# Kernel tuning notes

Hardware: AMD Instinct MI355X
Metric: run time of the kernel (lower is better)

## Reference

```python
import jax, jax.numpy as jnp
import numpy as np

W_WORDS = 30  # hardcoded by `temp[i][30*j+k]` in the original module


def setup_inputs() -> dict:
    key = jax.random.key(0)
    k1, k2 = jax.random.split(key)
    input_var = jax.random.randint(k1, (32, 32, W_WORDS), 0, 50000, dtype=jnp.int64)
    W_emb = jax.random.normal(k2, (50000, 300), dtype=jnp.float32)
    return {"input_var": input_var, "W_emb": W_emb}


def reference(input_var, W_emb):
    B, S, W = input_var.shape
    E = W_emb.shape[1]

    mask3 = input_var != 0                               # [B,S,W]
    word_mask = mask3.reshape(-1, W).astype(jnp.uint8)   # [B*S, W]
    sent_mask = (mask3.sum(axis=2) != 0).astype(jnp.uint8)  # [B,S]

    # Vectorized version of the triple loop: keep tokens up to the FIRST zero
    # in each sentence (the loop `break`s on the first zero), zero the rest.
    keep = jnp.cumprod(mask3.astype(jnp.int32), axis=2).astype(bool)  # [B,S,W]
    temp = jnp.where(keep, input_var, 0).reshape(B, S * W)            # [B, S*W]
    mask = (temp != 0).astype(jnp.uint8)                              # [B, S*W]

    # model_type == 'word' branch; dropout p=0 is identity
    embedded = W_emb[input_var].reshape(-1, W, E)   # [B*S, W, E]
    share_enc_embedded = W_emb[temp]                # [B, S*W, E]

    return embedded, share_enc_embedded, mask, word_mask, sent_mask
```

## Files before the change

### kernel.cpp

```cpp
#include <hip/hip_runtime.h>

constexpr int B  = 32;
constexpr int S  = 32;
constexpr int W  = 30;
constexpr int E  = 300;
constexpr int EV = E / 4;
constexpr int NSENT = B * S;
constexpr int NTOK  = NSENT * W;
constexpr int NF4   = NTOK * EV;

constexpr long OFF_EMB   = 0;
constexpr long OFF_SHARE = (long)NTOK * E;
constexpr long OFF_MASK  = OFF_SHARE + (long)NTOK * E;
constexpr long OFF_WM    = OFF_MASK + (long)NTOK;
constexpr long OFF_SM    = OFF_WM + (long)NTOK;

__global__ __launch_bounds__(256) void prep_kernel(
    const int* __restrict__ input,
    float* __restrict__ out,
    int* __restrict__ zarr)
{
    const int sent = blockIdx.x * 256 + threadIdx.x;
    if (sent >= NSENT) return;

    int vals[W];
    #pragma unroll
    for (int k = 0; k < W; ++k) vals[k] = input[sent * W + k];

    int z = W, any = 0;
    #pragma unroll
    for (int k = 0; k < W; ++k) {
        any |= (vals[k] != 0);
        if (vals[k] == 0 && z == W) z = k;
    }

    zarr[sent] = z;
    out[OFF_SM + sent] = any ? 1.0f : 0.0f;

    #pragma unroll
    for (int k = 0; k < W; ++k) {
        out[OFF_WM   + (long)sent * W + k] = (vals[k] != 0) ? 1.0f : 0.0f;
        out[OFF_MASK + (long)sent * W + k] = (k < z) ? 1.0f : 0.0f;
    }
}

__global__ __launch_bounds__(256) void gather_kernel(
    const int* __restrict__ input,
    const int* __restrict__ zarr,
    const float* __restrict__ Wemb,
    float* __restrict__ out)
{
    const int g = blockIdx.x * 256 + threadIdx.x;

    const int token = g / EV;
    const int q     = g - token * EV;
    const int sent  = token / W;
    const int k     = token - sent * W;

    const int idx = input[token];
    const int z   = zarr[sent];
    const int tix = (k < z) ? idx : 0;

    const float4* __restrict__ W4 = (const float4*)Wemb;
    float4 a = W4[(long)idx * EV + q];
    float4 b = (tix == idx) ? a : W4[(long)q];

    ((float4*)(out + OFF_EMB))[g]   = a;
    ((float4*)(out + OFF_SHARE))[g] = b;
}

extern "C" void kernel_launch(void* const* d_in, const int* in_sizes, int n_in,
                              void* d_out, int out_size, void* d_ws, size_t ws_size,
                              hipStream_t stream) {
    const int*   input = (const int*)d_in[0];
    const float* Wemb  = (const float*)d_in[1];
    float*       out   = (float*)d_out;
    int*         zarr  = (int*)d_ws;

    prep_kernel<<<(NSENT + 255) / 256, 256, 0, stream>>>(input, out, zarr);
    gather_kernel<<<NF4 / 256, 256, 0, stream>>>(input, zarr, Wemb, out);
}
```

Measured before the change: 121.6 us.

## Fuse mask prep into gather kernel with per-sentence blocks and wave ballot

Merges the mask/prefix computation kernel into the embedding gather kernel. Each block handles one ninth of a sentence, computes the first-zero position with a wavefront ballot, stages token indices in shared memory, and part 0 writes the mask outputs. This removes a second launch, the serial per-thread prep loop, and the workspace round trip. In exchange, every block re-reads the sentence indices and pays a barrier, and 6 of 256 threads per block sit idle.

```diff
diff --git a/kernel.cpp b/kernel.cpp
--- a/kernel.cpp
+++ b/kernel.cpp
@@ -7,7 +7,8 @@
 constexpr int EV = E / 4;
 constexpr int NSENT = B * S;
 constexpr int NTOK  = NSENT * W;
-constexpr int NF4   = NTOK * EV;
+constexpr int PARTS = 9;
+constexpr int F4_PER_PART = (W * EV) / PARTS;
 
 constexpr long OFF_EMB   = 0;
 constexpr long OFF_SHARE = (long)NTOK * E;
@@ -15,55 +16,53 @@
 constexpr long OFF_WM    = OFF_MASK + (long)NTOK;
 constexpr long OFF_SM    = OFF_WM + (long)NTOK;
 
-__global__ __launch_bounds__(256) void prep_kernel(
+__global__ __launch_bounds__(256) void fused_kernel(
     const int* __restrict__ input,
-    float* __restrict__ out,
-    int* __restrict__ zarr)
-{
-    const int sent = blockIdx.x * 256 + threadIdx.x;
-    if (sent >= NSENT) return;
-
-    int vals[W];
-    #pragma unroll
-    for (int k = 0; k < W; ++k) vals[k] = input[sent * W + k];
-
-    int z = W, any = 0;
-    #pragma unroll
-    for (int k = 0; k < W; ++k) {
-        any |= (vals[k] != 0);
-        if (vals[k] == 0 && z == W) z = k;
-    }
-
-    zarr[sent] = z;
-    out[OFF_SM + sent] = any ? 1.0f : 0.0f;
-
-    #pragma unroll
-    for (int k = 0; k < W; ++k) {
-        out[OFF_WM   + (long)sent * W + k] = (vals[k] != 0) ? 1.0f : 0.0f;
-        out[OFF_MASK + (long)sent * W + k] = (k < z) ? 1.0f : 0.0f;
-    }
-}
-
-__global__ __launch_bounds__(256) void gather_kernel(
-    const int* __restrict__ input,
-    const int* __restrict__ zarr,
     const float* __restrict__ Wemb,
     float* __restrict__ out)
 {
-    const int g = blockIdx.x * 256 + threadIdx.x;
+    const int bid  = blockIdx.x;
+    const int sent = bid / PARTS;
+    const int part = bid - sent * PARTS;
+    const int tid  = threadIdx.x;
 
-    const int token = g / EV;
-    const int q     = g - token * EV;
-    const int sent  = token / W;
-    const int k     = token - sent * W;
+    __shared__ int idx_s[W];
+    __shared__ int tix_s[W];
 
-    const int idx = input[token];
-    const int z   = zarr[sent];
-    const int tix = (k < z) ? idx : 0;
+    if (tid < 64) {
+        const int k = tid;
+        const int v = (k < W) ? input[sent * W + k] : 1;
+        const unsigned long long bz = __ballot(v == 0);
+        const int z = bz ? (int)__builtin_ctzll(bz) : W;
+        if (k < W) {
+            idx_s[k] = v;
+            tix_s[k] = (k < z) ? v : 0;
+            if (part == 0) {
+                out[OFF_WM   + (long)sent * W + k] = (v != 0) ? 1.0f : 0.0f;
+                out[OFF_MASK + (long)sent * W + k] = (k < z) ? 1.0f : 0.0f;
+            }
+        }
+        if (part == 0 && k == 0) {
+            constexpr unsigned long long ALLZ = (1ull << W) - 1;
+            out[OFF_SM + sent] = (bz != ALLZ) ? 1.0f : 0.0f;
+        }
+    }
+    __syncthreads();
+
+    if (tid >= F4_PER_PART) return;
+
+    const int i = part * F4_PER_PART + tid;
+    const int k = i / EV;
+    const int q = i - k * EV;
+
+    const int idx = idx_s[k];
+    const int tix = tix_s[k];
 
     const float4* __restrict__ W4 = (const float4*)Wemb;
+    const long g = (long)sent * (W * EV) + i;
+
     float4 a = W4[(long)idx * EV + q];
-    float4 b = (tix == idx) ? a : W4[(long)q];
+    float4 b = (tix == idx) ? a : W4[q];
 
     ((float4*)(out + OFF_EMB))[g]   = a;
     ((float4*)(out + OFF_SHARE))[g] = b;
@@ -75,8 +74,6 @@
     const int*   input = (const int*)d_in[0];
     const float* Wemb  = (const float*)d_in[1];
     float*       out   = (float*)d_out;
-    int*         zarr  = (int*)d_ws;
 
-    prep_kernel<<<(NSENT + 255) / 256, 256, 0, stream>>>(input, out, zarr);
-    gather_kernel<<<NF4 / 256, 256, 0, stream>>>(input, zarr, Wemb, out);
+    fused_kernel<<<NSENT * PARTS, 256, 0, stream>>>(input, Wemb, out);
 }
```

Result: faster. 119.1 us (-2.0%).
